# Optimization experiments

Measured on AMD Instinct MI355X. Metric: run time of the kernel, lower is better.

## Reference

```python
import jax, jax.numpy as jnp
import numpy as np

NPOINT, RADIUS, NSAMPLE = 512, 0.2, 32
EPS = 1e-5
CHANNELS = [67, 64, 64, 128]


def _fps(pts, npoint):
    # pts: [B, N, 3]; deterministic start at index 0 (torch impl uses randint)
    B, N, _ = pts.shape
    def body(carry, _):
        mind, far = carry
        c = jnp.take_along_axis(pts, far[:, None, None], axis=1)         # [B,1,3]
        mind = jnp.minimum(mind, jnp.sum((pts - c) ** 2, axis=-1))
        return (mind, jnp.argmax(mind, axis=-1).astype(jnp.int32)), far
    init = (jnp.full((B, N), 1e10, pts.dtype), jnp.zeros((B,), jnp.int32))
    _, idxs = jax.lax.scan(body, init, None, length=npoint)
    return idxs.T                                                         # [B, npoint]


def _gather(p, idx):
    # p: [B, N, C], idx: [B, ...] -> [B, ..., C]
    return jax.vmap(lambda pp, ii: pp[ii])(p, idx)


def _cbr(x, w, b, g, be, m, v):
    # Conv3d kernel [1, 4, 1]; torch padding='same' on even kernel -> (lo=1, hi=2) on t axis
    y = jax.lax.conv_general_dilated(x, w, (1, 1, 1),
                                     [(0, 0), (1, 2), (0, 0)],
                                     dimension_numbers=('NCDHW', 'OIDHW', 'NCDHW'))
    ex = lambda a: a[None, :, None, None, None]
    y = y + ex(b)
    # BatchNorm3d (eval mode with running stats)
    y = (y - ex(m)) * ex(g / jnp.sqrt(v + EPS)) + ex(be)
    return jax.nn.relu(y)


def _forward(xyz, points, params):
    B, t, _, N = xyz.shape
    S, K = NPOINT, NSAMPLE
    xf = jnp.transpose(xyz, (0, 1, 3, 2)).reshape(B * t, N, 3)            # [BT,N,3]
    pf = jnp.transpose(points, (0, 1, 3, 2)).reshape(B * t, N, -1)        # [BT,N,D]
    fidx = _fps(xf.reshape(B, t, N, 3)[:, 0], S)                          # [B,S], FPS on frame 0
    fidx_bt = jnp.broadcast_to(fidx[:, None, :], (B, t, S)).reshape(B * t, S)
    new_xyz = _gather(xf, fidx_bt)                                        # [BT,S,3]
    # squared distances via matmul form (matches square_distance)
    sq = (jnp.sum(new_xyz ** 2, -1)[:, :, None] + jnp.sum(xf ** 2, -1)[:, None, :]
          - 2.0 * jnp.einsum('bsc,bnc->bsn', new_xyz, xf))                # [BT,S,N]
    # ball query: invalid -> N, sort indices, take first K, fallback to first valid
    gidx = jnp.where(sq > RADIUS ** 2, N, jnp.arange(N, dtype=jnp.int32)[None, None, :])
    gidx = jnp.sort(gidx, axis=-1)[:, :, :K]                              # [BT,S,K]
    gidx = jnp.where(gidx == N, gidx[:, :, :1], gidx)
    gxyz = _gather(xf, gidx) - new_xyz[:, :, None, :]                     # [BT,S,K,3]
    feat = jnp.concatenate([gxyz, _gather(pf, gidx)], axis=-1)            # [BT,S,K,3+D]
    feat = feat.reshape(B, t, S, K, -1).transpose(0, 4, 2, 1, 3)          # [B,C,S,t,K]
    for p in params:
        feat = _cbr(feat, *p)
    feat = jnp.max(feat, axis=-1)                                         # [B,C',S,t]
    new_points = jnp.transpose(feat, (0, 3, 1, 2))                        # [B,t,C',S]
    new_xyz = new_xyz.reshape(B, t, S, 3).transpose(0, 1, 3, 2)           # [B,t,3,S]
    return new_xyz, new_points


def setup_inputs() -> dict:
    key = jax.random.key(0)
    ks = jax.random.split(key, 40)
    B, t, D, N = 2, 8, 64, 1024
    inp = {
        'xyz': jax.random.uniform(ks[0], (B, t, 3, N), jnp.float32),
        'points': jax.random.normal(ks[1], (B, t, D, N), jnp.float32),
    }
    j = 2
    for i in range(3):
        ci, co = CHANNELS[i], CHANNELS[i + 1]
        inp[f'w{i}'] = jax.random.normal(ks[j], (co, ci, 1, 4, 1), jnp.float32) * 0.05; j += 1
        inp[f'b{i}'] = jax.random.normal(ks[j], (co,), jnp.float32) * 0.01; j += 1
        inp[f'g{i}'] = jax.random.uniform(ks[j], (co,), jnp.float32, 0.5, 1.5); j += 1
        inp[f'be{i}'] = jax.random.normal(ks[j], (co,), jnp.float32) * 0.1; j += 1
        inp[f'm{i}'] = jax.random.normal(ks[j], (co,), jnp.float32) * 0.1; j += 1
        inp[f'v{i}'] = jax.random.uniform(ks[j], (co,), jnp.float32, 0.5, 1.5); j += 1
    return inp


def reference(xyz, points, w0, b0, g0, be0, m0, v0, w1, b1, g1, be1, m1, v1, w2, b2, g2, be2, m2, v2):
    params = [(w0, b0, g0, be0, m0, v0), (w1, b1, g1, be1, m1, v1), (w2, b2, g2, be2, m2, v2)]
    return _forward(xyz, points, params)
```

## Files before the change

### kernel.cpp

```cpp
#include <hip/hip_runtime.h>
#include <math.h>

#define NPTS 1024
#define S_   512
#define T_   8
#define K_   32
#define B_   2

typedef short bf16x8 __attribute__((ext_vector_type(8)));
typedef short short4v __attribute__((ext_vector_type(4)));
typedef float f32x4 __attribute__((ext_vector_type(4)));
typedef float vf2 __attribute__((ext_vector_type(2)));

static __device__ __forceinline__ short f2bf(float f) {
    unsigned u = __float_as_uint(f);
    unsigned r = (u + 0x7FFFu + ((u >> 16) & 1u)) >> 16;
    return (short)r;
}

template <int CTRL>
static __device__ __forceinline__ float dppmaxf(float x) {
    int mv = __builtin_amdgcn_update_dpp(0, __float_as_int(x), CTRL, 0xF, 0xF, true);
    return fmaxf(x, __int_as_float(mv));
}
static __device__ __forceinline__ unsigned wavemax_bits_f(float x) {
    x = dppmaxf<0x111>(x); x = dppmaxf<0x112>(x);
    x = dppmaxf<0x114>(x); x = dppmaxf<0x118>(x);
    x = dppmaxf<0x142>(x); x = dppmaxf<0x143>(x);
    return (unsigned)__builtin_amdgcn_readlane(__float_as_int(x), 63);
}

static __device__ __forceinline__ vf2 pk_sub(vf2 a, vf2 b) { return a - b; }
static __device__ __forceinline__ vf2 pk_fma(vf2 a, vf2 b, vf2 c) {
#if __has_builtin(__builtin_elementwise_fma)
    return __builtin_elementwise_fma(a, b, c);
#else
    vf2 r; r[0] = __fmaf_rn(a[0], b[0], c[0]); r[1] = __fmaf_rn(a[1], b[1], c[1]); return r;
#endif
}
static __device__ __forceinline__ vf2 pk_min(vf2 a, vf2 b) {
#if __has_builtin(__builtin_elementwise_min)
    return __builtin_elementwise_min(a, b);
#else
    vf2 r; r[0] = fminf(a[0], b[0]); r[1] = fminf(a[1], b[1]); return r;
#endif
}
static __device__ __forceinline__ vf2 pk_max(vf2 a, vf2 b) {
#if __has_builtin(__builtin_elementwise_max)
    return __builtin_elementwise_max(a, b);
#else
    vf2 r; r[0] = fmaxf(a[0], b[0]); r[1] = fmaxf(a[1], b[1]); return r;
#endif
}

__global__ __launch_bounds__(64) void fps_kernel(const float* __restrict__ xyz,
                                                 int* __restrict__ fidx)
{
    int b    = blockIdx.x;
    int lane = threadIdx.x;
    __shared__ float4 sc[NPTS];
    const float* bx = xyz + (size_t)b * (T_ * 3 * NPTS);
    vf2 px2[8], py2[8], pz2[8], mind2[8];
#pragma unroll
    for (int q = 0; q < 4; ++q) {
        float4 vx = ((const float4*)(bx))[lane * 4 + q];
        float4 vy = ((const float4*)(bx + NPTS))[lane * 4 + q];
        float4 vz = ((const float4*)(bx + 2 * NPTS))[lane * 4 + q];
        px2[q*2]   = (vf2){vx.x, vx.y};  px2[q*2+1] = (vf2){vx.z, vx.w};
        py2[q*2]   = (vf2){vy.x, vy.y};  py2[q*2+1] = (vf2){vy.z, vy.w};
        pz2[q*2]   = (vf2){vz.x, vz.y};  pz2[q*2+1] = (vf2){vz.z, vz.w};
        int n0 = lane * 16 + q * 4;
        sc[n0+0] = make_float4(vx.x, vy.x, vz.x, 0.f);
        sc[n0+1] = make_float4(vx.y, vy.y, vz.y, 0.f);
        sc[n0+2] = make_float4(vx.z, vy.z, vz.z, 0.f);
        sc[n0+3] = make_float4(vx.w, vy.w, vz.w, 0.f);
        mind2[q*2] = (vf2){1e10f, 1e10f}; mind2[q*2+1] = (vf2){1e10f, 1e10f};
    }
    __syncthreads();

    int far = 0;
    for (int it = 0; it < S_; ++it) {
        if (lane == 0) fidx[b * S_ + it] = far;
        float4 c = sc[far];
        vf2 c2x = (vf2){c.x, c.x}, c2y = (vf2){c.y, c.y}, c2z = (vf2){c.z, c.z};
#pragma unroll
        for (int q = 0; q < 8; ++q) {
            vf2 dx = pk_sub(px2[q], c2x);
            vf2 dy = pk_sub(py2[q], c2y);
            vf2 dz = pk_sub(pz2[q], c2z);
            vf2 d  = pk_fma(dz, dz, pk_fma(dy, dy, dx * dx));
            mind2[q] = pk_min(mind2[q], d);
        }
        vf2 t4a = pk_max(mind2[0], mind2[4]);
        vf2 t4b = pk_max(mind2[1], mind2[5]);
        vf2 t4c = pk_max(mind2[2], mind2[6]);
        vf2 t4d = pk_max(mind2[3], mind2[7]);
        vf2 t2a = pk_max(t4a, t4c);
        vf2 t2b = pk_max(t4b, t4d);
        vf2 t1  = pk_max(t2a, t2b);
        float lmax = fmaxf(t1[0], t1[1]);
        unsigned maxb = wavemax_bits_f(lmax);
        int cj[16];
#pragma unroll
        for (int j = 0; j < 16; ++j)
            cj[j] = (__float_as_uint(mind2[j >> 1][j & 1]) == maxb) ? j : 64;
        int m8[8], m4[4], m2v[2];
#pragma unroll
        for (int j = 0; j < 8; ++j) m8[j] = min(cj[j], cj[j + 8]);
#pragma unroll
        for (int j = 0; j < 4; ++j) m4[j] = min(m8[j], m8[j + 4]);
        m2v[0] = min(m4[0], m4[2]); m2v[1] = min(m4[1], m4[3]);
        int minj = min(m2v[0], m2v[1]);
        unsigned long long mk = __ballot(minj < 64);
        int l0 = __ffsll((long long)mk) - 1;
        int jw = __builtin_amdgcn_readlane(minj, l0);
        far = l0 * 16 + jw;
    }
}

__global__ __launch_bounds__(256) void transpose_points(
    const float* __restrict__ pts, short* __restrict__ ptsT)
{
    int nt = blockIdx.x;
    int bt = blockIdx.y;
    __shared__ float tile[64][65];
    int tid = threadIdx.x;
    for (int e = tid; e < 4096; e += 256) {
        int ci = e >> 6, nn = e & 63;
        tile[ci][nn] = pts[((size_t)bt * 64 + ci) * NPTS + nt * 64 + nn];
    }
    __syncthreads();
    for (int e = tid; e < 4096; e += 256) {
        int nn = e >> 6, ci = e & 63;
        ptsT[((size_t)bt * NPTS + nt * 64 + nn) * 64 + ci] = f2bf(tile[ci][nn]);
    }
}

__global__ __launch_bounds__(256) void prep_all(
    const float* __restrict__ w0, const float* __restrict__ w1,
    const float* __restrict__ w2,
    short* __restrict__ wg0, short* __restrict__ wg1, short* __restrict__ wg2)
{
    int z = blockIdx.y;
    int e = blockIdx.x * 256 + threadIdx.x;
    if (z == 0) {
        const int CI = 67, CIp = 100, CO = 64;
        if (e >= 4 * CO * CIp) return;
        int dt = e / (CO * CIp);
        int rem = e - dt * (CO * CIp);
        int co = rem / CIp;
        int ci = rem - co * CIp;
        float val = 0.0f;
        int cref = (ci < 64) ? (ci + 3) : ((ci < 67) ? (ci - 64) : -1);
        if (cref >= 0) val = w0[((size_t)co * CI + cref) * 4 + dt];
        wg0[e] = f2bf(val);
    } else if (z == 1) {
        const int CI = 64, CIp = 72, CO = 64;
        if (e >= 4 * CO * CIp) return;
        int dt = e / (CO * CIp);
        int rem = e - dt * (CO * CIp);
        int co = rem / CIp;
        int ci = rem - co * CIp;
        wg1[e] = f2bf((ci < CI) ? w1[((size_t)co * CI + ci) * 4 + dt] : 0.0f);
    } else {
        const int CI = 64, CIp = 72, CO = 128;
        if (e >= 4 * CO * CIp) return;
        int dt = e / (CO * CIp);
        int rem = e - dt * (CO * CIp);
        int co = rem / CIp;
        int ci = rem - co * CIp;
        wg2[e] = f2bf((ci < CI) ? w2[((size_t)co * CI + ci) * 4 + dt] : 0.0f);
    }
}

__global__ __launch_bounds__(256) void conv123(
    const float* __restrict__ xyz, const short* __restrict__ ptsT,
    const int* __restrict__ fidx,
    const short* __restrict__ wg0, const float* __restrict__ bb0,
    const float* __restrict__ gg0, const float* __restrict__ be0,
    const float* __restrict__ mm0, const float* __restrict__ vv0,
    const short* __restrict__ wg1, const float* __restrict__ bb1,
    const float* __restrict__ gg1, const float* __restrict__ be1,
    const float* __restrict__ mm1, const float* __restrict__ vv1,
    const short* __restrict__ wg2, const float* __restrict__ bb2,
    const float* __restrict__ gg2, const float* __restrict__ be2,
    const float* __restrict__ mm2, const float* __restrict__ vv2,
    float* __restrict__ out0, float* __restrict__ outPool)
{
    const int CIp1 = 100, NK1 = 3;
    const int CIp2 = 72,  NK2 = 2;
    __shared__ __align__(16) short xsA[256 * CIp1];
    __shared__ int   gidx_l[8][K_];
    __shared__ float nxyz_l[8][3];
    short* xsB = xsA;

    int s = blockIdx.x, b = blockIdx.y;
    int tid = threadIdx.x;
    int lane = tid & 63;
    int wv   = tid >> 6;
    int l16  = lane & 15;
    int lq   = lane >> 4;

    int fid = fidx[b * S_ + s];
    for (int half = 0; half < 2; ++half) {
        int tt = wv * 2 + half;
        int bt = b * T_ + tt;
        const float* bx = xyz + (size_t)bt * 3 * NPTS;
        float nx = bx[fid], ny = bx[NPTS + fid], nz = bx[2 * NPTS + fid];
        if (lane < 3) {
            float vvv = (lane == 0) ? nx : ((lane == 1) ? ny : nz);
            out0[(bt * 3 + lane) * S_ + s] = vvv;
            nxyz_l[tt][lane] = vvv;
        }
        float A = __fmaf_rn(nz, nz, __fmaf_rn(ny, ny, __fmul_rn(nx, nx)));
        const float R2 = (float)(0.2 * 0.2);
        int count = 0, firstIdx = -1;
#pragma unroll
        for (int j = 0; j < 16; ++j) {
            int n = j * 64 + lane;
            float x = bx[n], y = bx[NPTS + n], z = bx[2 * NPTS + n];
            float Bn = __fmaf_rn(z, z, __fmaf_rn(y, y, __fmul_rn(x, x)));
            float C  = __fmaf_rn(nz, z, __fmaf_rn(ny, y, __fmul_rn(nx, x)));
            float sq = __fsub_rn(__fadd_rn(A, Bn), __fmul_rn(2.0f, C));
            bool valid = !(sq > R2);
            unsigned long long mb = __ballot(valid);
            if (valid) {
                int pos = count + __popcll(mb & ((1ull << lane) - 1ull));
                if (pos < K_) gidx_l[tt][pos] = n;
            }
            if (firstIdx < 0 && mb) firstIdx = j * 64 + (__ffsll((long long)mb) - 1);
            count += __popcll(mb);
        }
        if (count < K_) {
            for (int p = count + lane; p < K_; p += 64) gidx_l[tt][p] = firstIdx;
        }
    }
    __syncthreads();

    {
        int col = tid;
        int k = col & 31, tt = col >> 5;
        int bt = b * T_ + tt;
        short* xrow = &xsA[col * CIp1];
        int idx = gidx_l[tt][k];
        const short* prow = ptsT + ((size_t)bt * NPTS + idx) * 64;
#pragma unroll
        for (int c = 0; c < 8; ++c)
            ((int4*)xrow)[c] = ((const int4*)prow)[c];
#pragma unroll
        for (int ci = 0; ci < 3; ++ci)
            xrow[64 + ci] = f2bf(xyz[(size_t)(bt * 3 + ci) * NPTS + idx] - nxyz_l[tt][ci]);
        for (int ci = 67; ci < CIp1; ++ci) xrow[ci] = 0;
    }
    __syncthreads();

    {
        f32x4 acc[16];
#pragma unroll
        for (int nb = 0; nb < 16; ++nb) acc[nb] = (f32x4){0.f, 0.f, 0.f, 0.f};
#pragma unroll
        for (int ks = 0; ks < NK1; ++ks) {
            bf16x8 afr[4];
#pragma unroll
            for (int dt = 0; dt < 4; ++dt)
                afr[dt] = *(const bf16x8*)&wg0[((size_t)(dt * 64 + wv * 16 + l16)) * CIp1 + ks * 32 + lq * 8];
            bf16x8 bfr[16];
#pragma unroll
            for (int cb = 0; cb < 16; ++cb)
                bfr[cb] = *(const bf16x8*)&xsA[(cb * 16 + l16) * CIp1 + ks * 32 + lq * 8];
#pragma unroll
            for (int dt = 0; dt < 4; ++dt) {
#pragma unroll
                for (int nb = 0; nb < 16; ++nb) {
                    int cb = nb + (dt - 1) * 2;
                    if (cb >= 0 && cb < 16)
                        acc[nb] = __builtin_amdgcn_mfma_f32_16x16x32_bf16(
                            afr[dt], bfr[cb], acc[nb], 0, 0, 0);
                }
            }
        }
        __syncthreads();
        float sc[4], c2[4];
#pragma unroll
        for (int j = 0; j < 4; ++j) {
            int co = wv * 16 + lq * 4 + j;
            float scv = gg0[co] / sqrtf(vv0[co] + 1e-5f);
            sc[j] = scv;
            c2[j] = (bb0[co] - mm0[co]) * scv + be0[co];
        }
#pragma unroll
        for (int nb = 0; nb < 16; ++nb) {
            int col = nb * 16 + l16;
            short4v pk;
#pragma unroll
            for (int j = 0; j < 4; ++j)
                pk[j] = f2bf(fmaxf(acc[nb][j] * sc[j] + c2[j], 0.0f));
            *(short4v*)&xsB[col * CIp2 + wv * 16 + lq * 4] = pk;
        }
        *(int4*)&xsB[tid * CIp2 + 64] = make_int4(0, 0, 0, 0);
    }
    __syncthreads();

    {
        f32x4 acc[16];
#pragma unroll
        for (int nb = 0; nb < 16; ++nb) acc[nb] = (f32x4){0.f, 0.f, 0.f, 0.f};
#pragma unroll
        for (int ks = 0; ks < NK2; ++ks) {
            bf16x8 afr[4];
#pragma unroll
            for (int dt = 0; dt < 4; ++dt)
                afr[dt] = *(const bf16x8*)&wg1[((size_t)(dt * 64 + wv * 16 + l16)) * CIp2 + ks * 32 + lq * 8];
            bf16x8 bfr[16];
#pragma unroll
            for (int cb = 0; cb < 16; ++cb)
                bfr[cb] = *(const bf16x8*)&xsB[(cb * 16 + l16) * CIp2 + ks * 32 + lq * 8];
#pragma unroll
            for (int dt = 0; dt < 4; ++dt) {
#pragma unroll
                for (int nb = 0; nb < 16; ++nb) {
                    int cb = nb + (dt - 1) * 2;
                    if (cb >= 0 && cb < 16)
                        acc[nb] = __builtin_amdgcn_mfma_f32_16x16x32_bf16(
                            afr[dt], bfr[cb], acc[nb], 0, 0, 0);
                }
            }
        }
        __syncthreads();
        float sc[4], c2[4];
#pragma unroll
        for (int j = 0; j < 4; ++j) {
            int co = wv * 16 + lq * 4 + j;
            float scv = gg1[co] / sqrtf(vv1[co] + 1e-5f);
            sc[j] = scv;
            c2[j] = (bb1[co] - mm1[co]) * scv + be1[co];
        }
#pragma unroll
        for (int nb = 0; nb < 16; ++nb) {
            int col = nb * 16 + l16;
            short4v pk;
#pragma unroll
            for (int j = 0; j < 4; ++j)
                pk[j] = f2bf(fmaxf(acc[nb][j] * sc[j] + c2[j], 0.0f));
            *(short4v*)&xsB[col * CIp2 + wv * 16 + lq * 4] = pk;
        }
    }
    __syncthreads();

#pragma unroll
    for (int st = 0; st < 2; ++st) {
        f32x4 acc[16];
#pragma unroll
        for (int nb = 0; nb < 16; ++nb) acc[nb] = (f32x4){0.f, 0.f, 0.f, 0.f};
#pragma unroll
        for (int ks = 0; ks < NK2; ++ks) {
            bf16x8 afr[4];
#pragma unroll
            for (int dt = 0; dt < 4; ++dt)
                afr[dt] = *(const bf16x8*)&wg2[((size_t)(dt * 128 + st * 64 + wv * 16 + l16)) * CIp2 + ks * 32 + lq * 8];
            bf16x8 bfr[16];
#pragma unroll
            for (int cb = 0; cb < 16; ++cb)
                bfr[cb] = *(const bf16x8*)&xsB[(cb * 16 + l16) * CIp2 + ks * 32 + lq * 8];
#pragma unroll
            for (int dt = 0; dt < 4; ++dt) {
#pragma unroll
                for (int nb = 0; nb < 16; ++nb) {
                    int cb = nb + (dt - 1) * 2;
                    if (cb >= 0 && cb < 16)
                        acc[nb] = __builtin_amdgcn_mfma_f32_16x16x32_bf16(
                            afr[dt], bfr[cb], acc[nb], 0, 0, 0);
                }
            }
        }
        float sc[4], c2[4];
#pragma unroll
        for (int j = 0; j < 4; ++j) {
            int co = st * 64 + wv * 16 + lq * 4 + j;
            float scv = gg2[co] / sqrtf(vv2[co] + 1e-5f);
            sc[j] = scv;
            c2[j] = (bb2[co] - mm2[co]) * scv + be2[co];
        }
#pragma unroll
        for (int nbp = 0; nbp < 8; ++nbp) {
#pragma unroll
            for (int j = 0; j < 4; ++j) {
                float v0 = fmaxf(acc[2 * nbp][j] * sc[j] + c2[j], 0.0f);
                float v1 = fmaxf(acc[2 * nbp + 1][j] * sc[j] + c2[j], 0.0f);
                float v = fmaxf(v0, v1);
#pragma unroll
                for (int off = 1; off < 16; off <<= 1)
                    v = fmaxf(v, __shfl_xor(v, off));
                if (l16 == 0) {
                    int co = st * 64 + wv * 16 + lq * 4 + j;
                    outPool[((size_t)(b * T_ + nbp) * 128 + co) * S_ + s] = v;
                }
            }
        }
    }
}

extern "C" void kernel_launch(void* const* d_in, const int* in_sizes, int n_in,
                              void* d_out, int out_size, void* d_ws, size_t ws_size,
                              hipStream_t stream)
{
    (void)in_sizes; (void)n_in; (void)out_size; (void)ws_size;
    const float* xyz    = (const float*)d_in[0];
    const float* points = (const float*)d_in[1];
    const float* w0 = (const float*)d_in[2];
    const float* b0 = (const float*)d_in[3];
    const float* g0 = (const float*)d_in[4];
    const float* be0 = (const float*)d_in[5];
    const float* m0 = (const float*)d_in[6];
    const float* v0 = (const float*)d_in[7];
    const float* w1 = (const float*)d_in[8];
    const float* b1 = (const float*)d_in[9];
    const float* g1 = (const float*)d_in[10];
    const float* be1 = (const float*)d_in[11];
    const float* m1 = (const float*)d_in[12];
    const float* v1 = (const float*)d_in[13];
    const float* w2 = (const float*)d_in[14];
    const float* b2 = (const float*)d_in[15];
    const float* g2 = (const float*)d_in[16];
    const float* be2 = (const float*)d_in[17];
    const float* m2 = (const float*)d_in[18];
    const float* v2 = (const float*)d_in[19];

    float* out = (float*)d_out;
    char* ws = (char*)d_ws;
    int*   fidx = (int*)ws;
    short* wg0  = (short*)(ws + (size_t)(3 * 1024 * 1024));
    short* wg1  = (short*)(ws + (size_t)(3 * 1024 * 1024) + 256 * 1024);
    short* wg2  = (short*)(ws + (size_t)(3 * 1024 * 1024) + 512 * 1024);
    short* ptsT = (short*)(ws + (size_t)(4  * 1024 * 1024));

    prep_all<<<dim3(144, 3), 256, 0, stream>>>(w0, w1, w2, wg0, wg1, wg2);
    transpose_points<<<dim3(16, B_ * T_), 256, 0, stream>>>(points, ptsT);
    fps_kernel<<<B_, 64, 0, stream>>>(xyz, fidx);

    conv123<<<dim3(S_, B_), 256, 0, stream>>>(
        xyz, ptsT, fidx,
        wg0, b0, g0, be0, m0, v0,
        wg1, b1, g1, be1, m1, v1,
        wg2, b2, g2, be2, m2, v2,
        out, out + (size_t)B_ * T_ * 3 * S_);
}
```

Baseline: 355.0 us.

## Fuse FPS into conv kernel with flag-based producer/consumer streaming of indices

```diff
diff --git a/kernel.cpp b/kernel.cpp
--- a/kernel.cpp
+++ b/kernel.cpp
@@ -51,71 +51,6 @@
 #else
     vf2 r; r[0] = fmaxf(a[0], b[0]); r[1] = fmaxf(a[1], b[1]); return r;
 #endif
-}
-
-__global__ __launch_bounds__(64) void fps_kernel(const float* __restrict__ xyz,
-                                                 int* __restrict__ fidx)
-{
-    int b    = blockIdx.x;
-    int lane = threadIdx.x;
-    __shared__ float4 sc[NPTS];
-    const float* bx = xyz + (size_t)b * (T_ * 3 * NPTS);
-    vf2 px2[8], py2[8], pz2[8], mind2[8];
-#pragma unroll
-    for (int q = 0; q < 4; ++q) {
-        float4 vx = ((const float4*)(bx))[lane * 4 + q];
-        float4 vy = ((const float4*)(bx + NPTS))[lane * 4 + q];
-        float4 vz = ((const float4*)(bx + 2 * NPTS))[lane * 4 + q];
-        px2[q*2]   = (vf2){vx.x, vx.y};  px2[q*2+1] = (vf2){vx.z, vx.w};
-        py2[q*2]   = (vf2){vy.x, vy.y};  py2[q*2+1] = (vf2){vy.z, vy.w};
-        pz2[q*2]   = (vf2){vz.x, vz.y};  pz2[q*2+1] = (vf2){vz.z, vz.w};
-        int n0 = lane * 16 + q * 4;
-        sc[n0+0] = make_float4(vx.x, vy.x, vz.x, 0.f);
-        sc[n0+1] = make_float4(vx.y, vy.y, vz.y, 0.f);
-        sc[n0+2] = make_float4(vx.z, vy.z, vz.z, 0.f);
-        sc[n0+3] = make_float4(vx.w, vy.w, vz.w, 0.f);
-        mind2[q*2] = (vf2){1e10f, 1e10f}; mind2[q*2+1] = (vf2){1e10f, 1e10f};
-    }
-    __syncthreads();
-
-    int far = 0;
-    for (int it = 0; it < S_; ++it) {
-        if (lane == 0) fidx[b * S_ + it] = far;
-        float4 c = sc[far];
-        vf2 c2x = (vf2){c.x, c.x}, c2y = (vf2){c.y, c.y}, c2z = (vf2){c.z, c.z};
-#pragma unroll
-        for (int q = 0; q < 8; ++q) {
-            vf2 dx = pk_sub(px2[q], c2x);
-            vf2 dy = pk_sub(py2[q], c2y);
-            vf2 dz = pk_sub(pz2[q], c2z);
-            vf2 d  = pk_fma(dz, dz, pk_fma(dy, dy, dx * dx));
-            mind2[q] = pk_min(mind2[q], d);
-        }
-        vf2 t4a = pk_max(mind2[0], mind2[4]);
-        vf2 t4b = pk_max(mind2[1], mind2[5]);
-        vf2 t4c = pk_max(mind2[2], mind2[6]);
-        vf2 t4d = pk_max(mind2[3], mind2[7]);
-        vf2 t2a = pk_max(t4a, t4c);
-        vf2 t2b = pk_max(t4b, t4d);
-        vf2 t1  = pk_max(t2a, t2b);
-        float lmax = fmaxf(t1[0], t1[1]);
-        unsigned maxb = wavemax_bits_f(lmax);
-        int cj[16];
-#pragma unroll
-        for (int j = 0; j < 16; ++j)
-            cj[j] = (__float_as_uint(mind2[j >> 1][j & 1]) == maxb) ? j : 64;
-        int m8[8], m4[4], m2v[2];
-#pragma unroll
-        for (int j = 0; j < 8; ++j) m8[j] = min(cj[j], cj[j + 8]);
-#pragma unroll
-        for (int j = 0; j < 4; ++j) m4[j] = min(m8[j], m8[j + 4]);
-        m2v[0] = min(m4[0], m4[2]); m2v[1] = min(m4[1], m4[3]);
-        int minj = min(m2v[0], m2v[1]);
-        unsigned long long mk = __ballot(minj < 64);
-        int l0 = __ffsll((long long)mk) - 1;
-        int jw = __builtin_amdgcn_readlane(minj, l0);
-        far = l0 * 16 + jw;
-    }
 }
 
 __global__ __launch_bounds__(256) void transpose_points(
@@ -173,9 +108,12 @@
     }
 }
 
-__global__ __launch_bounds__(256) void conv123(
+#define NWORK 512
+#define SMEM_BYTES (256 * 100 * 2 + 8 * K_ * 4 + 8 * 3 * 4)
+
+__global__ __launch_bounds__(256) void mega(
     const float* __restrict__ xyz, const short* __restrict__ ptsT,
-    const int* __restrict__ fidx,
+    int* __restrict__ fidx,
     const short* __restrict__ wg0, const float* __restrict__ bb0,
     const float* __restrict__ gg0, const float* __restrict__ be0,
     const float* __restrict__ mm0, const float* __restrict__ vv0,
@@ -187,213 +125,299 @@
     const float* __restrict__ mm2, const float* __restrict__ vv2,
     float* __restrict__ out0, float* __restrict__ outPool)
 {
+    __shared__ __align__(16) char smem[SMEM_BYTES];
+    int tid = threadIdx.x;
+
+    if (blockIdx.x < 2) {
+        if (tid >= 64) return;
+        int b    = blockIdx.x;
+        int lane = tid;
+        float4* sc = (float4*)smem;
+        const float* bx = xyz + (size_t)b * (T_ * 3 * NPTS);
+        vf2 px2[8], py2[8], pz2[8], mind2[8];
+#pragma unroll
+        for (int q = 0; q < 4; ++q) {
+            float4 vx = ((const float4*)(bx))[lane * 4 + q];
+            float4 vy = ((const float4*)(bx + NPTS))[lane * 4 + q];
+            float4 vz = ((const float4*)(bx + 2 * NPTS))[lane * 4 + q];
+            px2[q*2]   = (vf2){vx.x, vx.y};  px2[q*2+1] = (vf2){vx.z, vx.w};
+            py2[q*2]   = (vf2){vy.x, vy.y};  py2[q*2+1] = (vf2){vy.z, vy.w};
+            pz2[q*2]   = (vf2){vz.x, vz.y};  pz2[q*2+1] = (vf2){vz.z, vz.w};
+            int n0 = lane * 16 + q * 4;
+            sc[n0+0] = make_float4(vx.x, vy.x, vz.x, 0.f);
+            sc[n0+1] = make_float4(vx.y, vy.y, vz.y, 0.f);
+            sc[n0+2] = make_float4(vx.z, vy.z, vz.z, 0.f);
+            sc[n0+3] = make_float4(vx.w, vy.w, vz.w, 0.f);
+            mind2[q*2] = (vf2){1e10f, 1e10f}; mind2[q*2+1] = (vf2){1e10f, 1e10f};
+        }
+        asm volatile("s_waitcnt lgkmcnt(0)" ::: "memory");
+
+        int far = 0;
+        for (int it = 0; it < S_; ++it) {
+            if (lane == 0)
+                __hip_atomic_store(&fidx[b * S_ + it], far + 1,
+                                   __ATOMIC_RELAXED, __HIP_MEMORY_SCOPE_AGENT);
+            float4 c = sc[far];
+            vf2 c2x = (vf2){c.x, c.x}, c2y = (vf2){c.y, c.y}, c2z = (vf2){c.z, c.z};
+#pragma unroll
+            for (int q = 0; q < 8; ++q) {
+                vf2 dx = pk_sub(px2[q], c2x);
+                vf2 dy = pk_sub(py2[q], c2y);
+                vf2 dz = pk_sub(pz2[q], c2z);
+                vf2 d  = pk_fma(dz, dz, pk_fma(dy, dy, dx * dx));
+                mind2[q] = pk_min(mind2[q], d);
+            }
+            vf2 t4a = pk_max(mind2[0], mind2[4]);
+            vf2 t4b = pk_max(mind2[1], mind2[5]);
+            vf2 t4c = pk_max(mind2[2], mind2[6]);
+            vf2 t4d = pk_max(mind2[3], mind2[7]);
+            vf2 t2a = pk_max(t4a, t4c);
+            vf2 t2b = pk_max(t4b, t4d);
+            vf2 t1  = pk_max(t2a, t2b);
+            float lmax = fmaxf(t1[0], t1[1]);
+            unsigned maxb = wavemax_bits_f(lmax);
+            int cj[16];
+#pragma unroll
+            for (int j = 0; j < 16; ++j)
+                cj[j] = (__float_as_uint(mind2[j >> 1][j & 1]) == maxb) ? j : 64;
+            int m8[8], m4[4], m2v[2];
+#pragma unroll
+            for (int j = 0; j < 8; ++j) m8[j] = min(cj[j], cj[j + 8]);
+#pragma unroll
+            for (int j = 0; j < 4; ++j) m4[j] = min(m8[j], m8[j + 4]);
+            m2v[0] = min(m4[0], m4[2]); m2v[1] = min(m4[1], m4[3]);
+            int minj = min(m2v[0], m2v[1]);
+            unsigned long long mk = __ballot(minj < 64);
+            int l0 = __ffsll((long long)mk) - 1;
+            int jw = __builtin_amdgcn_readlane(minj, l0);
+            far = l0 * 16 + jw;
+        }
+        return;
+    }
+
     const int CIp1 = 100, NK1 = 3;
     const int CIp2 = 72,  NK2 = 2;
-    __shared__ __align__(16) short xsA[256 * CIp1];
-    __shared__ int   gidx_l[8][K_];
-    __shared__ float nxyz_l[8][3];
-    short* xsB = xsA;
-
-    int s = blockIdx.x, b = blockIdx.y;
-    int tid = threadIdx.x;
+    short* xsA    = (short*)smem;
+    short* xsB    = xsA;
+    int*   gidx_l = (int*)(smem + 256 * 100 * 2);
+    float* nxyz_l = (float*)(smem + 256 * 100 * 2 + 8 * K_ * 4);
+
+    int w = blockIdx.x - 2;
     int lane = tid & 63;
     int wv   = tid >> 6;
     int l16  = lane & 15;
     int lq   = lane >> 4;
 
-    int fid = fidx[b * S_ + s];
-    for (int half = 0; half < 2; ++half) {
-        int tt = wv * 2 + half;
-        int bt = b * T_ + tt;
-        const float* bx = xyz + (size_t)bt * 3 * NPTS;
-        float nx = bx[fid], ny = bx[NPTS + fid], nz = bx[2 * NPTS + fid];
-        if (lane < 3) {
-            float vvv = (lane == 0) ? nx : ((lane == 1) ? ny : nz);
-            out0[(bt * 3 + lane) * S_ + s] = vvv;
-            nxyz_l[tt][lane] = vvv;
-        }
-        float A = __fmaf_rn(nz, nz, __fmaf_rn(ny, ny, __fmul_rn(nx, nx)));
-        const float R2 = (float)(0.2 * 0.2);
-        int count = 0, firstIdx = -1;
-#pragma unroll
-        for (int j = 0; j < 16; ++j) {
-            int n = j * 64 + lane;
-            float x = bx[n], y = bx[NPTS + n], z = bx[2 * NPTS + n];
-            float Bn = __fmaf_rn(z, z, __fmaf_rn(y, y, __fmul_rn(x, x)));
-            float C  = __fmaf_rn(nz, z, __fmaf_rn(ny, y, __fmul_rn(nx, x)));
-            float sq = __fsub_rn(__fadd_rn(A, Bn), __fmul_rn(2.0f, C));
-            bool valid = !(sq > R2);
-            unsigned long long mb = __ballot(valid);
-            if (valid) {
-                int pos = count + __popcll(mb & ((1ull << lane) - 1ull));
-                if (pos < K_) gidx_l[tt][pos] = n;
-            }
-            if (firstIdx < 0 && mb) firstIdx = j * 64 + (__ffsll((long long)mb) - 1);
-            count += __popcll(mb);
-        }
-        if (count < K_) {
-            for (int p = count + lane; p < K_; p += 64) gidx_l[tt][p] = firstIdx;
-        }
-    }
-    __syncthreads();
-
-    {
-        int col = tid;
-        int k = col & 31, tt = col >> 5;
-        int bt = b * T_ + tt;
-        short* xrow = &xsA[col * CIp1];
-        int idx = gidx_l[tt][k];
-        const short* prow = ptsT + ((size_t)bt * NPTS + idx) * 64;
-#pragma unroll
-        for (int c = 0; c < 8; ++c)
-            ((int4*)xrow)[c] = ((const int4*)prow)[c];
-#pragma unroll
-        for (int ci = 0; ci < 3; ++ci)
-            xrow[64 + ci] = f2bf(xyz[(size_t)(bt * 3 + ci) * NPTS + idx] - nxyz_l[tt][ci]);
-        for (int ci = 67; ci < CIp1; ++ci) xrow[ci] = 0;
-    }
-    __syncthreads();
-
-    {
-        f32x4 acc[16];
-#pragma unroll
-        for (int nb = 0; nb < 16; ++nb) acc[nb] = (f32x4){0.f, 0.f, 0.f, 0.f};
-#pragma unroll
-        for (int ks = 0; ks < NK1; ++ks) {
-            bf16x8 afr[4];
-#pragma unroll
-            for (int dt = 0; dt < 4; ++dt)
-                afr[dt] = *(const bf16x8*)&wg0[((size_t)(dt * 64 + wv * 16 + l16)) * CIp1 + ks * 32 + lq * 8];
-            bf16x8 bfr[16];
-#pragma unroll
-            for (int cb = 0; cb < 16; ++cb)
-                bfr[cb] = *(const bf16x8*)&xsA[(cb * 16 + l16) * CIp1 + ks * 32 + lq * 8];
-#pragma unroll
-            for (int dt = 0; dt < 4; ++dt) {
-#pragma unroll
-                for (int nb = 0; nb < 16; ++nb) {
-                    int cb = nb + (dt - 1) * 2;
-                    if (cb >= 0 && cb < 16)
-                        acc[nb] = __builtin_amdgcn_mfma_f32_16x16x32_bf16(
-                            afr[dt], bfr[cb], acc[nb], 0, 0, 0);
+    for (int jobi = 0; jobi < 2; ++jobi) {
+        int job = w + jobi * NWORK;
+        int s = job >> 1, b = job & 1;
+        __syncthreads();
+
+        int fid;
+        {
+            const int* p = &fidx[b * S_ + s];
+            int v = 0, guard = 0;
+            do {
+                v = __hip_atomic_load(p, __ATOMIC_RELAXED, __HIP_MEMORY_SCOPE_AGENT);
+                if (v) break;
+                __builtin_amdgcn_s_sleep(2);
+            } while (++guard < (1 << 24));
+            fid = v - 1;
+        }
+
+        for (int half = 0; half < 2; ++half) {
+            int tt = wv * 2 + half;
+            int bt = b * T_ + tt;
+            const float* bx = xyz + (size_t)bt * 3 * NPTS;
+            float nx = bx[fid], ny = bx[NPTS + fid], nz = bx[2 * NPTS + fid];
+            if (lane < 3) {
+                float vvv = (lane == 0) ? nx : ((lane == 1) ? ny : nz);
+                out0[(bt * 3 + lane) * S_ + s] = vvv;
+                nxyz_l[tt * 3 + lane] = vvv;
+            }
+            float A = __fmaf_rn(nz, nz, __fmaf_rn(ny, ny, __fmul_rn(nx, nx)));
+            const float R2 = (float)(0.2 * 0.2);
+            int count = 0, firstIdx = -1;
+#pragma unroll
+            for (int j = 0; j < 16; ++j) {
+                int n = j * 64 + lane;
+                float x = bx[n], y = bx[NPTS + n], z = bx[2 * NPTS + n];
+                float Bn = __fmaf_rn(z, z, __fmaf_rn(y, y, __fmul_rn(x, x)));
+                float C  = __fmaf_rn(nz, z, __fmaf_rn(ny, y, __fmul_rn(nx, x)));
+                float sq = __fsub_rn(__fadd_rn(A, Bn), __fmul_rn(2.0f, C));
+                bool valid = !(sq > R2);
+                unsigned long long mb = __ballot(valid);
+                if (valid) {
+                    int pos = count + __popcll(mb & ((1ull << lane) - 1ull));
+                    if (pos < K_) gidx_l[tt * K_ + pos] = n;
                 }
+                if (firstIdx < 0 && mb) firstIdx = j * 64 + (__ffsll((long long)mb) - 1);
+                count += __popcll(mb);
+            }
+            if (count < K_) {
+                for (int p = count + lane; p < K_; p += 64) gidx_l[tt * K_ + p] = firstIdx;
             }
         }
         __syncthreads();
-        float sc[4], c2[4];
-#pragma unroll
-        for (int j = 0; j < 4; ++j) {
-            int co = wv * 16 + lq * 4 + j;
-            float scv = gg0[co] / sqrtf(vv0[co] + 1e-5f);
-            sc[j] = scv;
-            c2[j] = (bb0[co] - mm0[co]) * scv + be0[co];
-        }
-#pragma unroll
-        for (int nb = 0; nb < 16; ++nb) {
-            int col = nb * 16 + l16;
-            short4v pk;
-#pragma unroll
-            for (int j = 0; j < 4; ++j)
-                pk[j] = f2bf(fmaxf(acc[nb][j] * sc[j] + c2[j], 0.0f));
-            *(short4v*)&xsB[col * CIp2 + wv * 16 + lq * 4] = pk;
-        }
-        *(int4*)&xsB[tid * CIp2 + 64] = make_int4(0, 0, 0, 0);
-    }
-    __syncthreads();
-
-    {
-        f32x4 acc[16];
-#pragma unroll
-        for (int nb = 0; nb < 16; ++nb) acc[nb] = (f32x4){0.f, 0.f, 0.f, 0.f};
-#pragma unroll
-        for (int ks = 0; ks < NK2; ++ks) {
-            bf16x8 afr[4];
-#pragma unroll
-            for (int dt = 0; dt < 4; ++dt)
-                afr[dt] = *(const bf16x8*)&wg1[((size_t)(dt * 64 + wv * 16 + l16)) * CIp2 + ks * 32 + lq * 8];
-            bf16x8 bfr[16];
-#pragma unroll
-            for (int cb = 0; cb < 16; ++cb)
-                bfr[cb] = *(const bf16x8*)&xsB[(cb * 16 + l16) * CIp2 + ks * 32 + lq * 8];
-#pragma unroll
-            for (int dt = 0; dt < 4; ++dt) {
-#pragma unroll
-                for (int nb = 0; nb < 16; ++nb) {
-                    int cb = nb + (dt - 1) * 2;
-                    if (cb >= 0 && cb < 16)
-                        acc[nb] = __builtin_amdgcn_mfma_f32_16x16x32_bf16(
-                            afr[dt], bfr[cb], acc[nb], 0, 0, 0);
+
+        {
+            int col = tid;
+            int k = col & 31, tt = col >> 5;
+            int bt = b * T_ + tt;
+            short* xrow = &xsA[col * CIp1];
+            int idx = gidx_l[tt * K_ + k];
+            const short* prow = ptsT + ((size_t)bt * NPTS + idx) * 64;
+#pragma unroll
+            for (int c = 0; c < 8; ++c)
+                ((int4*)xrow)[c] = ((const int4*)prow)[c];
+#pragma unroll
+            for (int ci = 0; ci < 3; ++ci)
+                xrow[64 + ci] = f2bf(xyz[(size_t)(bt * 3 + ci) * NPTS + idx] - nxyz_l[tt * 3 + ci]);
+            for (int ci = 67; ci < CIp1; ++ci) xrow[ci] = 0;
+        }
+        __syncthreads();
+
+        {
+            f32x4 acc[16];
+#pragma unroll
+            for (int nb = 0; nb < 16; ++nb) acc[nb] = (f32x4){0.f, 0.f, 0.f, 0.f};
+#pragma unroll
+            for (int ks = 0; ks < NK1; ++ks) {
+                bf16x8 afr[4];
+#pragma unroll
+                for (int dt = 0; dt < 4; ++dt)
+                    afr[dt] = *(const bf16x8*)&wg0[((size_t)(dt * 64 + wv * 16 + l16)) * CIp1 + ks * 32 + lq * 8];
+                bf16x8 bfr[16];
+#pragma unroll
+                for (int cb = 0; cb < 16; ++cb)
+                    bfr[cb] = *(const bf16x8*)&xsA[(cb * 16 + l16) * CIp1 + ks * 32 + lq * 8];
+#pragma unroll
+                for (int dt = 0; dt < 4; ++dt) {
+#pragma unroll
+                    for (int nb = 0; nb < 16; ++nb) {
+                        int cb = nb + (dt - 1) * 2;
+                        if (cb >= 0 && cb < 16)
+                            acc[nb] = __builtin_amdgcn_mfma_f32_16x16x32_bf16(
+                                afr[dt], bfr[cb], acc[nb], 0, 0, 0);
+                    }
                 }
             }
+            __syncthreads();
+            float sc0[4], c20[4];
+#pragma unroll
+            for (int j = 0; j < 4; ++j) {
+                int co = wv * 16 + lq * 4 + j;
+                float scv = gg0[co] / sqrtf(vv0[co] + 1e-5f);
+                sc0[j] = scv;
+                c20[j] = (bb0[co] - mm0[co]) * scv + be0[co];
+            }
+#pragma unroll
+            for (int nb = 0; nb < 16; ++nb) {
+                int col = nb * 16 + l16;
+                short4v pk;
+#pragma unroll
+                for (int j = 0; j < 4; ++j)
+                    pk[j] = f2bf(fmaxf(acc[nb][j] * sc0[j] + c20[j], 0.0f));
+                *(short4v*)&xsB[col * CIp2 + wv * 16 + lq * 4] = pk;
+            }
+            *(int4*)&xsB[tid * CIp2 + 64] = make_int4(0, 0, 0, 0);
         }
         __syncthreads();
-        float sc[4], c2[4];
-#pragma unroll
-        for (int j = 0; j < 4; ++j) {
-            int co = wv * 16 + lq * 4 + j;
-            float scv = gg1[co] / sqrtf(vv1[co] + 1e-5f);
-            sc[j] = scv;
-            c2[j] = (bb1[co] - mm1[co]) * scv + be1[co];
-        }
-#pragma unroll
-        for (int nb = 0; nb < 16; ++nb) {
-            int col = nb * 16 + l16;
-            short4v pk;
-#pragma unroll
-            for (int j = 0; j < 4; ++j)
-                pk[j] = f2bf(fmaxf(acc[nb][j] * sc[j] + c2[j], 0.0f));
-            *(short4v*)&xsB[col * CIp2 + wv * 16 + lq * 4] = pk;
-        }
-    }
-    __syncthreads();
-
-#pragma unroll
-    for (int st = 0; st < 2; ++st) {
-        f32x4 acc[16];
-#pragma unroll
-        for (int nb = 0; nb < 16; ++nb) acc[nb] = (f32x4){0.f, 0.f, 0.f, 0.f};
-#pragma unroll
-        for (int ks = 0; ks < NK2; ++ks) {
-            bf16x8 afr[4];
-#pragma unroll
-            for (int dt = 0; dt < 4; ++dt)
-                afr[dt] = *(const bf16x8*)&wg2[((size_t)(dt * 128 + st * 64 + wv * 16 + l16)) * CIp2 + ks * 32 + lq * 8];
-            bf16x8 bfr[16];
-#pragma unroll
-            for (int cb = 0; cb < 16; ++cb)
-                bfr[cb] = *(const bf16x8*)&xsB[(cb * 16 + l16) * CIp2 + ks * 32 + lq * 8];
-#pragma unroll
-            for (int dt = 0; dt < 4; ++dt) {
-#pragma unroll
-                for (int nb = 0; nb < 16; ++nb) {
-                    int cb = nb + (dt - 1) * 2;
-                    if (cb >= 0 && cb < 16)
-                        acc[nb] = __builtin_amdgcn_mfma_f32_16x16x32_bf16(
-                            afr[dt], bfr[cb], acc[nb], 0, 0, 0);
+
+        {
+            f32x4 acc[16];
+#pragma unroll
+            for (int nb = 0; nb < 16; ++nb) acc[nb] = (f32x4){0.f, 0.f, 0.f, 0.f};
+#pragma unroll
+            for (int ks = 0; ks < NK2; ++ks) {
+                bf16x8 afr[4];
+#pragma unroll
+                for (int dt = 0; dt < 4; ++dt)
+                    afr[dt] = *(const bf16x8*)&wg1[((size_t)(dt * 64 + wv * 16 + l16)) * CIp2 + ks * 32 + lq * 8];
+                bf16x8 bfr[16];
+#pragma unroll
+                for (int cb = 0; cb < 16; ++cb)
+                    bfr[cb] = *(const bf16x8*)&xsB[(cb * 16 + l16) * CIp2 + ks * 32 + lq * 8];
+#pragma unroll
+                for (int dt = 0; dt < 4; ++dt) {
+#pragma unroll
+                    for (int nb = 0; nb < 16; ++nb) {
+                        int cb = nb + (dt - 1) * 2;
+                        if (cb >= 0 && cb < 16)
+                            acc[nb] = __builtin_amdgcn_mfma_f32_16x16x32_bf16(
+                                afr[dt], bfr[cb], acc[nb], 0, 0, 0);
+                    }
                 }
             }
-        }
-        float sc[4], c2[4];
-#pragma unroll
-        for (int j = 0; j < 4; ++j) {
-            int co = st * 64 + wv * 16 + lq * 4 + j;
-            float scv = gg2[co] / sqrtf(vv2[co] + 1e-5f);
-            sc[j] = scv;
-            c2[j] = (bb2[co] - mm2[co]) * scv + be2[co];
-        }
-#pragma unroll
-        for (int nbp = 0; nbp < 8; ++nbp) {
+            __syncthreads();
+            float sc1[4], c21[4];
 #pragma unroll
             for (int j = 0; j < 4; ++j) {
-                float v0 = fmaxf(acc[2 * nbp][j] * sc[j] + c2[j], 0.0f);
-                float v1 = fmaxf(acc[2 * nbp + 1][j] * sc[j] + c2[j], 0.0f);
-                float v = fmaxf(v0, v1);
-#pragma unroll
-                for (int off = 1; off < 16; off <<= 1)
-                    v = fmaxf(v, __shfl_xor(v, off));
-                if (l16 == 0) {
-                    int co = st * 64 + wv * 16 + lq * 4 + j;
-                    outPool[((size_t)(b * T_ + nbp) * 128 + co) * S_ + s] = v;
+                int co = wv * 16 + lq * 4 + j;
+                float scv = gg1[co] / sqrtf(vv1[co] + 1e-5f);
+                sc1[j] = scv;
+                c21[j] = (bb1[co] - mm1[co]) * scv + be1[co];
+            }
+#pragma unroll
+            for (int nb = 0; nb < 16; ++nb) {
+                int col = nb * 16 + l16;
+                short4v pk;
+#pragma unroll
+                for (int j = 0; j < 4; ++j)
+                    pk[j] = f2bf(fmaxf(acc[nb][j] * sc1[j] + c21[j], 0.0f));
+                *(short4v*)&xsB[col * CIp2 + wv * 16 + lq * 4] = pk;
+            }
+        }
+        __syncthreads();
+
+#pragma unroll
+        for (int st = 0; st < 2; ++st) {
+            f32x4 acc[16];
+#pragma unroll
+            for (int nb = 0; nb < 16; ++nb) acc[nb] = (f32x4){0.f, 0.f, 0.f, 0.f};
+#pragma unroll
+            for (int ks = 0; ks < NK2; ++ks) {
+                bf16x8 afr[4];
+#pragma unroll
+                for (int dt = 0; dt < 4; ++dt)
+                    afr[dt] = *(const bf16x8*)&wg2[((size_t)(dt * 128 + st * 64 + wv * 16 + l16)) * CIp2 + ks * 32 + lq * 8];
+                bf16x8 bfr[16];
+#pragma unroll
+                for (int cb = 0; cb < 16; ++cb)
+                    bfr[cb] = *(const bf16x8*)&xsB[(cb * 16 + l16) * CIp2 + ks * 32 + lq * 8];
+#pragma unroll
+                for (int dt = 0; dt < 4; ++dt) {
+#pragma unroll
+                    for (int nb = 0; nb < 16; ++nb) {
+                        int cb = nb + (dt - 1) * 2;
+                        if (cb >= 0 && cb < 16)
+                            acc[nb] = __builtin_amdgcn_mfma_f32_16x16x32_bf16(
+                                afr[dt], bfr[cb], acc[nb], 0, 0, 0);
+                    }
+                }
+            }
+            float sc2[4], c22[4];
+#pragma unroll
+            for (int j = 0; j < 4; ++j) {
+                int co = st * 64 + wv * 16 + lq * 4 + j;
+                float scv = gg2[co] / sqrtf(vv2[co] + 1e-5f);
+                sc2[j] = scv;
+                c22[j] = (bb2[co] - mm2[co]) * scv + be2[co];
+            }
+#pragma unroll
+            for (int nbp = 0; nbp < 8; ++nbp) {
+#pragma unroll
+                for (int j = 0; j < 4; ++j) {
+                    float v0 = fmaxf(acc[2 * nbp][j] * sc2[j] + c22[j], 0.0f);
+                    float v1 = fmaxf(acc[2 * nbp + 1][j] * sc2[j] + c22[j], 0.0f);
+                    float v = fmaxf(v0, v1);
+#pragma unroll
+                    for (int off = 1; off < 16; off <<= 1)
+                        v = fmaxf(v, __shfl_xor(v, off));
+                    if (l16 == 0) {
+                        int co = st * 64 + wv * 16 + lq * 4 + j;
+                        outPool[((size_t)(b * T_ + nbp) * 128 + co) * S_ + s] = v;
+                    }
                 }
             }
         }
@@ -434,11 +458,11 @@
     short* wg2  = (short*)(ws + (size_t)(3 * 1024 * 1024) + 512 * 1024);
     short* ptsT = (short*)(ws + (size_t)(4  * 1024 * 1024));
 
+    hipMemsetAsync(fidx, 0, B_ * S_ * sizeof(int), stream);
     prep_all<<<dim3(144, 3), 256, 0, stream>>>(w0, w1, w2, wg0, wg1, wg2);
     transpose_points<<<dim3(16, B_ * T_), 256, 0, stream>>>(points, ptsT);
-    fps_kernel<<<B_, 64, 0, stream>>>(xyz, fidx);
-
-    conv123<<<dim3(S_, B_), 256, 0, stream>>>(
+
+    mega<<<dim3(2 + NWORK), 256, 0, stream>>>(
         xyz, ptsT, fidx,
         wg0, b0, g0, be0, m0, v0,
         wg1, b1, g1, be1, m1, v1,
```

Measured after the change: 292.6 us. 1.21x faster.
